# Optimization experiments

Measured on AMD Instinct MI355X. Metric: run time of the kernel, lower is better.

## Reference

```python
import jax, jax.numpy as jnp
import numpy as np

D_MODEL = 1024
N_HEADS = 16
HEAD_DIM = D_MODEL // N_HEADS
B, T = 4, 2048


def setup_inputs() -> dict:
    key = jax.random.key(0)
    ks = jax.random.split(key, 5)
    s = 1.0 / np.sqrt(D_MODEL)
    return {
        "x": jax.random.normal(ks[0], (B, T, D_MODEL), dtype=jnp.float32),
        "Wq": jax.random.normal(ks[1], (D_MODEL, D_MODEL), dtype=jnp.float32) * s,
        "bq": jnp.zeros((D_MODEL,), jnp.float32),
        "Wk": jax.random.normal(ks[2], (D_MODEL, D_MODEL), dtype=jnp.float32) * s,
        "bk": jnp.zeros((D_MODEL,), jnp.float32),
        "Wv": jax.random.normal(ks[3], (D_MODEL, D_MODEL), dtype=jnp.float32) * s,
        "bv": jnp.zeros((D_MODEL,), jnp.float32),
        "Wo": jax.random.normal(ks[4], (D_MODEL, D_MODEL), dtype=jnp.float32) * s,
        "bo": jnp.zeros((D_MODEL,), jnp.float32),
    }


def reference(x, Wq, bq, Wk, bk, Wv, bv, Wo, bo):
    Bx, Tx, C = x.shape
    H, Dh = N_HEADS, HEAD_DIM
    # projections (torch Linear: y = x @ W.T + b)
    q = (x @ Wq.T + bq).reshape(Bx, Tx, H, Dh).transpose(0, 2, 1, 3)  # [B,H,T,Dh]
    k = (x @ Wk.T + bk).reshape(Bx, Tx, H, Dh).transpose(0, 2, 1, 3)
    v = (x @ Wv.T + bv).reshape(Bx, Tx, H, Dh).transpose(0, 2, 1, 3)
    scores = jnp.einsum("bhqd,bhkd->bhqk", q, k) / np.sqrt(Dh).astype(np.float32)
    causal = jnp.tril(jnp.ones((Tx, Tx), dtype=bool))
    scores = jnp.where(causal, scores, -jnp.inf)
    attn = jax.nn.softmax(scores, axis=-1)  # dropout in eval mode = identity
    y = jnp.einsum("bhqk,bhkd->bhqd", attn, v)
    y = y.transpose(0, 2, 1, 3).reshape(Bx, Tx, C)
    return y @ Wo.T + bo
```

## Files before the change

### kernel.cpp

```cpp
#include <hip/hip_runtime.h>

typedef __attribute__((ext_vector_type(8))) short short8;
typedef __attribute__((ext_vector_type(4))) float f32x4;
typedef unsigned short u16;
typedef unsigned int u32;

#define NH 16

#if __has_builtin(__builtin_amdgcn_exp2f)
#define EXP2(x) __builtin_amdgcn_exp2f(x)
#else
#define EXP2(x) exp2f(x)
#endif

__device__ __forceinline__ u32 f2bf(float f) {
  u32 u = __builtin_bit_cast(u32, f);
  return (u + 0x7fffu + ((u >> 16) & 1u)) >> 16;
}

__global__ __launch_bounds__(256) void k_convert(
    const float* __restrict__ x, const float* __restrict__ wq,
    const float* __restrict__ wk, const float* __restrict__ wv,
    const float* __restrict__ wo, u16* __restrict__ dst) {
  int i = blockIdx.x * 256 + threadIdx.x;
  size_t e = (size_t)i * 4;
  const float* s; size_t off;
  if (e < 8388608ull)       { s = x;  off = e; }
  else if (e < 9437184ull)  { s = wq; off = e - 8388608ull; }
  else if (e < 10485760ull) { s = wk; off = e - 9437184ull; }
  else if (e < 11534336ull) { s = wv; off = e - 10485760ull; }
  else                      { s = wo; off = e - 11534336ull; }
  float4 d = *(const float4*)(s + off);
  ushort4 o;
  o.x = (u16)f2bf(d.x); o.y = (u16)f2bf(d.y);
  o.z = (u16)f2bf(d.z); o.w = (u16)f2bf(d.w);
  *(ushort4*)(dst + e) = o;
}

#define GEMM_CORE(Aptr, Bptr)                                                   \
  __shared__ u16 As[128 * 72];                                                  \
  __shared__ u16 Bs[128 * 72];                                                  \
  const int tid = threadIdx.x;                                                  \
  const int wave = tid >> 6, lane = tid & 63;                                   \
  const int wr = wave >> 1, wc = wave & 1;                                      \
  const int quad = lane >> 4, l16 = lane & 15;                                  \
  const int m0 = blockIdx.y * 128, n0 = blockIdx.x * 128;                       \
  f32x4 acc[4][4];                                                              \
  {                                                                             \
    f32x4 z = {0.f, 0.f, 0.f, 0.f};                                             \
    for (int a = 0; a < 4; ++a) for (int b2 = 0; b2 < 4; ++b2) acc[a][b2] = z;  \
  }                                                                             \
  for (int k0 = 0; k0 < 1024; k0 += 64) {                                       \
    _Pragma("unroll")                                                           \
    for (int i = 0; i < 4; ++i) {                                               \
      int c = i * 256 + tid;                                                    \
      int row = c >> 3, cc = c & 7;                                             \
      *(uint4*)(&As[row * 72 + cc * 8]) =                                       \
          *(const uint4*)(Aptr + (size_t)(m0 + row) * 1024 + k0 + cc * 8);      \
      *(uint4*)(&Bs[row * 72 + cc * 8]) =                                       \
          *(const uint4*)(Bptr + (size_t)(n0 + row) * 1024 + k0 + cc * 8);      \
    }                                                                           \
    __syncthreads();                                                            \
    _Pragma("unroll")                                                           \
    for (int ks = 0; ks < 2; ++ks) {                                            \
      short8 af[4], bfr[4];                                                     \
      _Pragma("unroll")                                                         \
      for (int t = 0; t < 4; ++t)                                               \
        af[t] = *(const short8*)(&As[(wr * 64 + t * 16 + l16) * 72 + ks * 32 + quad * 8]); \
      _Pragma("unroll")                                                         \
      for (int t = 0; t < 4; ++t)                                               \
        bfr[t] = *(const short8*)(&Bs[(wc * 64 + t * 16 + l16) * 72 + ks * 32 + quad * 8]); \
      _Pragma("unroll")                                                         \
      for (int mt = 0; mt < 4; ++mt) {                                          \
        _Pragma("unroll")                                                       \
        for (int nt = 0; nt < 4; ++nt)                                          \
          acc[mt][nt] = __builtin_amdgcn_mfma_f32_16x16x32_bf16(                \
              af[mt], bfr[nt], acc[mt][nt], 0, 0, 0);                           \
      }                                                                         \
    }                                                                           \
    __syncthreads();                                                            \
  }

__global__ __launch_bounds__(256, 2) void k_gemm_qkv(
    const u16* __restrict__ A, const u16* __restrict__ W,
    const float* __restrict__ bq, const float* __restrict__ bk,
    const float* __restrict__ bv, u16* __restrict__ qkv) {
  const int z = blockIdx.z;
  const u16* Bw = W + (size_t)z * 1048576;
  const float* bias = (z == 0) ? bq : (z == 1) ? bk : bv;
  u16* out = qkv + (size_t)z * 8388608;
  GEMM_CORE(A, Bw)
  const float scl = (z == 0) ? 0.125f * 1.44269504088896340736f : 1.0f;
  #pragma unroll
  for (int mt = 0; mt < 4; ++mt) {
    #pragma unroll
    for (int nt = 0; nt < 4; ++nt) {
      int n = n0 + wc * 64 + nt * 16 + l16;
      float bn = bias[n];
      int h = n >> 6, d = n & 63;
      #pragma unroll
      for (int r = 0; r < 4; ++r) {
        int m = m0 + wr * 64 + mt * 16 + quad * 4 + r;
        int b = m >> 11, t = m & 2047;
        float val = (acc[mt][nt][r] + bn) * scl;
        out[(((size_t)(b * NH + h) * 2048 + t) << 6) + d] = (u16)f2bf(val);
      }
    }
  }
}

__global__ __launch_bounds__(256, 2) void k_gemm_out(
    const u16* __restrict__ A, const u16* __restrict__ Bw,
    const float* __restrict__ bias, float* __restrict__ out) {
  GEMM_CORE(A, Bw)
  #pragma unroll
  for (int mt = 0; mt < 4; ++mt) {
    #pragma unroll
    for (int nt = 0; nt < 4; ++nt) {
      int n = n0 + wc * 64 + nt * 16 + l16;
      float bn = bias[n];
      #pragma unroll
      for (int r = 0; r < 4; ++r) {
        int m = m0 + wr * 64 + mt * 16 + quad * 4 + r;
        out[(size_t)m * 1024 + n] = acc[mt][nt][r] + bn;
      }
    }
  }
}

__global__ __launch_bounds__(256) void k_vtrans(const u16* __restrict__ v,
                                                u16* __restrict__ vt) {
  int t0 = blockIdx.x * 64;
  int bh = blockIdx.y;
  const u16* vs = v + (size_t)bh * 2048 * 64;
  u16* vd = vt + (size_t)bh * 64 * 2048;
  int tid = threadIdx.x;
  #pragma unroll
  for (int it = 0; it < 2; ++it) {
    int c = it * 256 + tid;
    int d = c >> 3, tc = c & 7;
    u16 tmp[8];
    #pragma unroll
    for (int j = 0; j < 8; ++j)
      tmp[j] = vs[(size_t)(t0 + tc * 8 + j) * 64 + d];
    uint4 pk;
    pk.x = (u32)tmp[0] | ((u32)tmp[1] << 16);
    pk.y = (u32)tmp[2] | ((u32)tmp[3] << 16);
    pk.z = (u32)tmp[4] | ((u32)tmp[5] << 16);
    pk.w = (u32)tmp[6] | ((u32)tmp[7] << 16);
    *(uint4*)(vd + (size_t)d * 2048 + t0 + tc * 8) = pk;
  }
}


#define ATTN_SUB(P, QF0, QF1, O, MI, LI, DIAG)                                 \
  {                                                                            \
    f32x4 st[4];                                                               \
    _Pragma("unroll")                                                          \
    for (int nt = 0; nt < 4; ++nt) {                                           \
      short8 kf0 = *(const short8*)(&Ks[P][(nt * 16 + l16) * 72 + quad * 8]);  \
      short8 kf1 = *(const short8*)(&Ks[P][(nt * 16 + l16) * 72 + 32 + quad * 8]); \
      f32x4 z4 = {0.f, 0.f, 0.f, 0.f};                                         \
      z4 = __builtin_amdgcn_mfma_f32_16x16x32_bf16(kf0, QF0, z4, 0, 0, 0);     \
      st[nt] = __builtin_amdgcn_mfma_f32_16x16x32_bf16(kf1, QF1, z4, 0, 0, 0); \
    }                                                                          \
    if (DIAG) {                                                                \
      int q_loc = wave * 16 + l16;                                             \
      _Pragma("unroll")                                                        \
      for (int nt = 0; nt < 4; ++nt) {                                         \
        _Pragma("unroll")                                                      \
        for (int r = 0; r < 4; ++r) {                                          \
          int k_loc = nt * 16 + quad * 4 + r;                                  \
          if (k_loc > q_loc) st[nt][r] = -1e30f;                               \
        }                                                                      \
      }                                                                        \
    }                                                                          \
    float mq[4];                                                               \
    _Pragma("unroll")                                                          \
    for (int nt = 0; nt < 4; ++nt)                                             \
      mq[nt] = fmaxf(fmaxf(st[nt][0], st[nt][1]), fmaxf(st[nt][2], st[nt][3]));\
    float mx = fmaxf(fmaxf(mq[0], mq[1]), fmaxf(mq[2], mq[3]));                \
    mx = fmaxf(mx, __shfl_xor(mx, 16, 64));                                    \
    mx = fmaxf(mx, __shfl_xor(mx, 32, 64));                                    \
    float mnew = fmaxf(MI, mx);                                                \
    float alpha = EXP2(MI - mnew);                                             \
    MI = mnew;                                                                 \
    LI *= alpha;                                                               \
    _Pragma("unroll")                                                          \
    for (int r = 0; r < 4; ++r) {                                              \
      float av = __shfl(alpha, quad * 4 + r, 16);                              \
      _Pragma("unroll")                                                        \
      for (int dt = 0; dt < 4; ++dt) O[dt][r] *= av;                           \
    }                                                                          \
    u32 Wx[4], Wy[4];                                                          \
    float sq[4];                                                               \
    _Pragma("unroll")                                                          \
    for (int nt = 0; nt < 4; ++nt) {                                           \
      float p0 = EXP2(st[nt][0] - mnew);                                       \
      float p1 = EXP2(st[nt][1] - mnew);                                       \
      float p2 = EXP2(st[nt][2] - mnew);                                       \
      float p3 = EXP2(st[nt][3] - mnew);                                       \
      sq[nt] = (p0 + p1) + (p2 + p3);                                          \
      Wx[nt] = f2bf(p0) | (f2bf(p1) << 16);                                    \
      Wy[nt] = f2bf(p2) | (f2bf(p3) << 16);                                    \
    }                                                                          \
    float sum = (sq[0] + sq[1]) + (sq[2] + sq[3]);                             \
    sum += __shfl_xor(sum, 16, 64);                                            \
    sum += __shfl_xor(sum, 32, 64);                                            \
    LI += sum;                                                                 \
    uint4 t0, t1;                                                              \
    {                                                                          \
      u32 e, f;                                                                \
      e = __shfl(Wx[0], s0, 64); f = __shfl(Wx[1], s0, 64); t0.x = hi ? f : e; \
      e = __shfl(Wy[0], s0, 64); f = __shfl(Wy[1], s0, 64); t0.y = hi ? f : e; \
      e = __shfl(Wx[0], s1, 64); f = __shfl(Wx[1], s1, 64); t0.z = hi ? f : e; \
      e = __shfl(Wy[0], s1, 64); f = __shfl(Wy[1], s1, 64); t0.w = hi ? f : e; \
      e = __shfl(Wx[2], s0, 64); f = __shfl(Wx[3], s0, 64); t1.x = hi ? f : e; \
      e = __shfl(Wy[2], s0, 64); f = __shfl(Wy[3], s0, 64); t1.y = hi ? f : e; \
      e = __shfl(Wx[2], s1, 64); f = __shfl(Wx[3], s1, 64); t1.z = hi ? f : e; \
      e = __shfl(Wy[2], s1, 64); f = __shfl(Wy[3], s1, 64); t1.w = hi ? f : e; \
    }                                                                          \
    short8 pf0 = __builtin_bit_cast(short8, t0);                               \
    short8 pf1 = __builtin_bit_cast(short8, t1);                               \
    _Pragma("unroll")                                                          \
    for (int dt = 0; dt < 4; ++dt) {                                           \
      short8 vf0 = *(const short8*)(&Vs[P][(dt * 16 + l16) * 72 + quad * 8]);  \
      short8 vf1 = *(const short8*)(&Vs[P][(dt * 16 + l16) * 72 + 32 + quad * 8]); \
      O[dt] = __builtin_amdgcn_mfma_f32_16x16x32_bf16(pf0, vf0, O[dt], 0, 0, 0); \
      O[dt] = __builtin_amdgcn_mfma_f32_16x16x32_bf16(pf1, vf1, O[dt], 0, 0, 0); \
    }                                                                          \
  }

#define ATTN_EPI(O, LI, QT)                                                    \
  _Pragma("unroll")                                                            \
  for (int r = 0; r < 4; ++r) {                                                \
    float lv = __shfl(LI, quad * 4 + r, 16);                                   \
    float inv = 1.0f / lv;                                                     \
    int t = (QT) * 64 + wave * 16 + quad * 4 + r;                              \
    _Pragma("unroll")                                                          \
    for (int dt = 0; dt < 4; ++dt) {                                           \
      int d = dt * 16 + l16;                                                   \
      y[(((size_t)b * 2048 + t) * NH + h) * 64 + d] = (u16)f2bf(O[dt][r] * inv); \
    }                                                                          \
  }

__global__ __launch_bounds__(256, 4) void k_attn(
    const u16* __restrict__ q, const u16* __restrict__ k,
    const u16* __restrict__ vt, u16* __restrict__ y) {
  const int tid = threadIdx.x;
  const int wave = tid >> 6, lane = tid & 63;
  const int quad = lane >> 4, l16 = lane & 15;
  const int bh = blockIdx.x, bx = blockIdx.y;
  const int qtB = bx, qtA = 31 - bx;
  const int b = bh >> 4, h = bh & 15;

  __shared__ u16 Ks[2][64 * 72];
  __shared__ u16 Vs[2][64 * 72];

  const u16* qbA = q + ((size_t)bh * 2048 + qtA * 64 + wave * 16 + l16) * 64;
  short8 qA0 = *(const short8*)(qbA + quad * 8);
  short8 qA1 = *(const short8*)(qbA + 32 + quad * 8);
  const u16* qbB = q + ((size_t)bh * 2048 + qtB * 64 + wave * 16 + l16) * 64;
  short8 qB0 = *(const short8*)(qbB + quad * 8);
  short8 qB1 = *(const short8*)(qbB + 32 + quad * 8);

  f32x4 oA[4], oB[4];
  {
    f32x4 z = {0.f, 0.f, 0.f, 0.f};
    #pragma unroll
    for (int dt = 0; dt < 4; ++dt) { oA[dt] = z; oB[dt] = z; }
  }
  float mA = -1e30f, lA = 0.f, mB = -1e30f, lB = 0.f;

  const u16* kbase = k + (size_t)bh * 131072;
  const u16* vbase = vt + (size_t)bh * 131072;
  const int r0 = tid >> 3, cc = tid & 7;
  const int s0 = ((quad & 1) << 5) + l16, s1 = s0 + 16;
  const int hi = quad >> 1;

  {
    uint4 k0 = *(const uint4*)(kbase + (size_t)r0 * 64 + cc * 8);
    uint4 k1 = *(const uint4*)(kbase + (size_t)(r0 + 32) * 64 + cc * 8);
    uint4 v0 = *(const uint4*)(vbase + (size_t)r0 * 2048 + cc * 8);
    uint4 v1 = *(const uint4*)(vbase + (size_t)(r0 + 32) * 2048 + cc * 8);
    *(uint4*)(&Ks[0][r0 * 72 + cc * 8]) = k0;
    *(uint4*)(&Ks[0][(r0 + 32) * 72 + cc * 8]) = k1;
    *(uint4*)(&Vs[0][r0 * 72 + cc * 8]) = v0;
    *(uint4*)(&Vs[0][(r0 + 32) * 72 + cc * 8]) = v1;
  }
  __syncthreads();

  for (int kt = 0; kt <= qtA; ++kt) {
    const int p = kt & 1;
    const bool pre = (kt < qtA);
    uint4 kr0, kr1, vr0, vr1;
    if (pre) {
      const u16* kb = kbase + (size_t)(kt + 1) * 4096;
      const u16* vb = vbase + (kt + 1) * 64;
      kr0 = *(const uint4*)(kb + (size_t)r0 * 64 + cc * 8);
      kr1 = *(const uint4*)(kb + (size_t)(r0 + 32) * 64 + cc * 8);
      vr0 = *(const uint4*)(vb + (size_t)r0 * 2048 + cc * 8);
      vr1 = *(const uint4*)(vb + (size_t)(r0 + 32) * 2048 + cc * 8);
    }

    ATTN_SUB(p, qA0, qA1, oA, mA, lA, (kt == qtA))
    if (kt <= qtB) {
      ATTN_SUB(p, qB0, qB1, oB, mB, lB, (kt == qtB))
    }

    if (pre) {
      *(uint4*)(&Ks[p ^ 1][r0 * 72 + cc * 8]) = kr0;
      *(uint4*)(&Ks[p ^ 1][(r0 + 32) * 72 + cc * 8]) = kr1;
      *(uint4*)(&Vs[p ^ 1][r0 * 72 + cc * 8]) = vr0;
      *(uint4*)(&Vs[p ^ 1][(r0 + 32) * 72 + cc * 8]) = vr1;
    }
    __syncthreads();
  }

  ATTN_EPI(oA, lA, qtA)
  ATTN_EPI(oB, lB, qtB)
}

extern "C" void kernel_launch(void* const* d_in, const int* in_sizes, int n_in,
                              void* d_out, int out_size, void* d_ws, size_t ws_size,
                              hipStream_t stream) {
  const float* x  = (const float*)d_in[0];
  const float* Wq = (const float*)d_in[1];
  const float* bq = (const float*)d_in[2];
  const float* Wk = (const float*)d_in[3];
  const float* bk = (const float*)d_in[4];
  const float* Wv = (const float*)d_in[5];
  const float* bv = (const float*)d_in[6];
  const float* Wo = (const float*)d_in[7];
  const float* bo = (const float*)d_in[8];
  float* out = (float*)d_out;

  u16* ws  = (u16*)d_ws;
  u16* xb  = ws;
  u16* Wb  = ws + 8388608;
  u16* qkv = ws + 12582912;
  u16* vt  = ws + 37748736;
  u16* y   = ws + 46137344;

  k_convert<<<dim3(12288), dim3(256), 0, stream>>>(x, Wq, Wk, Wv, Wo, ws);
  k_gemm_qkv<<<dim3(8, 64, 3), dim3(256), 0, stream>>>(xb, Wb, bq, bk, bv, qkv);
  k_vtrans<<<dim3(32, 64), dim3(256), 0, stream>>>(qkv + 2 * 8388608, vt);
  k_attn<<<dim3(64, 16), dim3(256), 0, stream>>>(qkv, qkv + 8388608, vt, y);
  k_gemm_out<<<dim3(8, 64), dim3(256), 0, stream>>>(y, Wb + 3 * 1048576, bo, out);
}
```

Before: 309.1 us.

## Rewrite projection GEMMs with 256x256 tiles, async LDS loads and double buffering

Replaces the 128x128 register-staged GEMM core with a 256x256-tile, 8-wave kernel. It uses global_load_lds direct-to-LDS copies, double-buffered shared memory, XOR-swizzled LDS layout, and interleaved barrier/setprio phases so loads overlap MFMA work. The QKV projection becomes one fused N=3072 GEMM with a grouped block-index swizzle for L2 reuse. The goal is to cut global-load latency stalls and LDS bank conflicts, at the cost of 128KB LDS per block and fewer blocks (128 for the output GEMM), which may underfill the GPU.

New measurement: 321.4 us. 4.0% more time.

```diff
diff --git a/kernel.cpp b/kernel.cpp
--- a/kernel.cpp
+++ b/kernel.cpp
@@ -16,6 +16,12 @@
 __device__ __forceinline__ u32 f2bf(float f) {
   u32 u = __builtin_bit_cast(u32, f);
   return (u + 0x7fffu + ((u >> 16) & 1u)) >> 16;
+}
+
+__device__ __forceinline__ void gload_lds16(const u16* g, u16* l) {
+  __builtin_amdgcn_global_load_lds(
+      (const __attribute__((address_space(1))) void*)g,
+      (__attribute__((address_space(3))) void*)l, 16, 0, 0);
 }
 
 __global__ __launch_bounds__(256) void k_convert(
@@ -37,91 +43,184 @@
   *(ushort4*)(dst + e) = o;
 }
 
-#define GEMM_CORE(Aptr, Bptr)                                                   \
-  __shared__ u16 As[128 * 72];                                                  \
-  __shared__ u16 Bs[128 * 72];                                                  \
-  const int tid = threadIdx.x;                                                  \
-  const int wave = tid >> 6, lane = tid & 63;                                   \
-  const int wr = wave >> 1, wc = wave & 1;                                      \
-  const int quad = lane >> 4, l16 = lane & 15;                                  \
-  const int m0 = blockIdx.y * 128, n0 = blockIdx.x * 128;                       \
-  f32x4 acc[4][4];                                                              \
-  {                                                                             \
-    f32x4 z = {0.f, 0.f, 0.f, 0.f};                                             \
-    for (int a = 0; a < 4; ++a) for (int b2 = 0; b2 < 4; ++b2) acc[a][b2] = z;  \
-  }                                                                             \
-  for (int k0 = 0; k0 < 1024; k0 += 64) {                                       \
-    _Pragma("unroll")                                                           \
-    for (int i = 0; i < 4; ++i) {                                               \
-      int c = i * 256 + tid;                                                    \
-      int row = c >> 3, cc = c & 7;                                             \
-      *(uint4*)(&As[row * 72 + cc * 8]) =                                       \
-          *(const uint4*)(Aptr + (size_t)(m0 + row) * 1024 + k0 + cc * 8);      \
-      *(uint4*)(&Bs[row * 72 + cc * 8]) =                                       \
-          *(const uint4*)(Bptr + (size_t)(n0 + row) * 1024 + k0 + cc * 8);      \
-    }                                                                           \
-    __syncthreads();                                                            \
-    _Pragma("unroll")                                                           \
-    for (int ks = 0; ks < 2; ++ks) {                                            \
-      short8 af[4], bfr[4];                                                     \
-      _Pragma("unroll")                                                         \
-      for (int t = 0; t < 4; ++t)                                               \
-        af[t] = *(const short8*)(&As[(wr * 64 + t * 16 + l16) * 72 + ks * 32 + quad * 8]); \
-      _Pragma("unroll")                                                         \
-      for (int t = 0; t < 4; ++t)                                               \
-        bfr[t] = *(const short8*)(&Bs[(wc * 64 + t * 16 + l16) * 72 + ks * 32 + quad * 8]); \
-      _Pragma("unroll")                                                         \
-      for (int mt = 0; mt < 4; ++mt) {                                          \
-        _Pragma("unroll")                                                       \
-        for (int nt = 0; nt < 4; ++nt)                                          \
-          acc[mt][nt] = __builtin_amdgcn_mfma_f32_16x16x32_bf16(                \
-              af[mt], bfr[nt], acc[mt][nt], 0, 0, 0);                           \
-      }                                                                         \
-    }                                                                           \
-    __syncthreads();                                                            \
-  }
-
-__global__ __launch_bounds__(256, 2) void k_gemm_qkv(
+#define GEMM256_CORE(Aptr, Bptr)                                               \
+  __shared__ u16 As[2][16384];                                                 \
+  __shared__ u16 Bs[2][16384];                                                 \
+  const int tid = threadIdx.x;                                                 \
+  const int wave = tid >> 6, lane = tid & 63;                                  \
+  const int quad = lane >> 4, l16 = lane & 15;                                 \
+  const int wr = wave >> 2, wn = wave & 3;                                     \
+  const int swz = l16 & 7;                                                     \
+  const int srow = tid >> 3;                                                   \
+  const int srcg = (tid & 7) ^ (srow & 7);                                     \
+  const u16* aTh = Aptr + (size_t)(m0 + srow) * 1024 + srcg * 8;               \
+  const u16* bTh = Bptr + (size_t)(n0 + srow) * 1024 + srcg * 8;               \
+  u16* aDst = &As[0][0] + wave * 512;                                          \
+  u16* bDst = &Bs[0][0] + wave * 512;                                          \
+  f32x4 acc[8][4];                                                             \
+  {                                                                            \
+    f32x4 z = {0.f, 0.f, 0.f, 0.f};                                            \
+    for (int a = 0; a < 8; ++a) for (int b2 = 0; b2 < 4; ++b2) acc[a][b2] = z; \
+  }                                                                            \
+  _Pragma("unroll")                                                            \
+  for (int j = 0; j < 4; ++j) {                                                \
+    gload_lds16(aTh + j * 65536, aDst + j * 4096);                             \
+    gload_lds16(bTh + j * 65536, bDst + j * 4096);                             \
+  }                                                                            \
+  __syncthreads();                                                             \
+  for (int t = 0; t < 16; ++t) {                                               \
+    const int p = t & 1;                                                       \
+    if (t < 15) {                                                              \
+      const u16* aT = aTh + (t + 1) * 64;                                      \
+      const u16* bT = bTh + (t + 1) * 64;                                      \
+      u16* aD = aDst + (p ^ 1) * 16384;                                        \
+      u16* bD = bDst + (p ^ 1) * 16384;                                        \
+      _Pragma("unroll")                                                        \
+      for (int j = 0; j < 4; ++j) {                                            \
+        gload_lds16(aT + j * 65536, aD + j * 4096);                            \
+        gload_lds16(bT + j * 65536, bD + j * 4096);                            \
+      }                                                                        \
+    }                                                                          \
+    __builtin_amdgcn_sched_barrier(0);                                         \
+    const u16* Ab = &As[p][0];                                                 \
+    const u16* Bb = &Bs[p][0];                                                 \
+    short8 af[4][2], bfr[2][2];                                                \
+                                                            \
+    _Pragma("unroll")                                                          \
+    for (int mt = 0; mt < 4; ++mt)                                             \
+      _Pragma("unroll")                                                        \
+      for (int ks = 0; ks < 2; ++ks)                                           \
+        af[mt][ks] = *(const short8*)(Ab + (wr * 128 + mt * 16 + l16) * 64     \
+                                         + ((ks * 4 + quad) ^ swz) * 8);       \
+    _Pragma("unroll")                                                          \
+    for (int nt = 0; nt < 2; ++nt)                                             \
+      _Pragma("unroll")                                                        \
+      for (int ks = 0; ks < 2; ++ks)                                           \
+        bfr[nt][ks] = *(const short8*)(Bb + (wn * 64 + nt * 16 + l16) * 64     \
+                                          + ((ks * 4 + quad) ^ swz) * 8);      \
+    __builtin_amdgcn_s_barrier();                                              \
+    __builtin_amdgcn_s_setprio(1);                                             \
+    _Pragma("unroll")                                                          \
+    for (int mt = 0; mt < 4; ++mt)                                             \
+      _Pragma("unroll")                                                        \
+      for (int nt = 0; nt < 2; ++nt)                                           \
+        _Pragma("unroll")                                                      \
+        for (int ks = 0; ks < 2; ++ks)                                         \
+          acc[mt][nt] = __builtin_amdgcn_mfma_f32_16x16x32_bf16(               \
+              af[mt][ks], bfr[nt][ks], acc[mt][nt], 0, 0, 0);                  \
+    __builtin_amdgcn_s_setprio(0);                                             \
+    __builtin_amdgcn_s_barrier();                                              \
+    __builtin_amdgcn_sched_barrier(0);                                         \
+                                                  \
+    _Pragma("unroll")                                                          \
+    for (int nt = 0; nt < 2; ++nt)                                             \
+      _Pragma("unroll")                                                        \
+      for (int ks = 0; ks < 2; ++ks)                                           \
+        bfr[nt][ks] = *(const short8*)(Bb + (wn * 64 + (nt + 2) * 16 + l16) * 64 \
+                                          + ((ks * 4 + quad) ^ swz) * 8);      \
+    __builtin_amdgcn_s_barrier();                                              \
+    __builtin_amdgcn_s_setprio(1);                                             \
+    _Pragma("unroll")                                                          \
+    for (int mt = 0; mt < 4; ++mt)                                             \
+      _Pragma("unroll")                                                        \
+      for (int nt = 0; nt < 2; ++nt)                                           \
+        _Pragma("unroll")                                                      \
+        for (int ks = 0; ks < 2; ++ks)                                         \
+          acc[mt][nt + 2] = __builtin_amdgcn_mfma_f32_16x16x32_bf16(           \
+              af[mt][ks], bfr[nt][ks], acc[mt][nt + 2], 0, 0, 0);              \
+    __builtin_amdgcn_s_setprio(0);                                             \
+    __builtin_amdgcn_s_barrier();                                              \
+    __builtin_amdgcn_sched_barrier(0);                                         \
+                                                 \
+    _Pragma("unroll")                                                          \
+    for (int mt = 0; mt < 4; ++mt)                                             \
+      _Pragma("unroll")                                                        \
+      for (int ks = 0; ks < 2; ++ks)                                           \
+        af[mt][ks] = *(const short8*)(Ab + (wr * 128 + (mt + 4) * 16 + l16) * 64 \
+                                         + ((ks * 4 + quad) ^ swz) * 8);       \
+    __builtin_amdgcn_s_barrier();                                              \
+    __builtin_amdgcn_s_setprio(1);                                             \
+    _Pragma("unroll")                                                          \
+    for (int mt = 0; mt < 4; ++mt)                                             \
+      _Pragma("unroll")                                                        \
+      for (int nt = 0; nt < 2; ++nt)                                           \
+        _Pragma("unroll")                                                      \
+        for (int ks = 0; ks < 2; ++ks)                                         \
+          acc[mt + 4][nt + 2] = __builtin_amdgcn_mfma_f32_16x16x32_bf16(       \
+              af[mt][ks], bfr[nt][ks], acc[mt + 4][nt + 2], 0, 0, 0);          \
+    __builtin_amdgcn_s_setprio(0);                                             \
+    __builtin_amdgcn_s_barrier();                                              \
+    __builtin_amdgcn_sched_barrier(0);                                         \
+                                          \
+    _Pragma("unroll")                                                          \
+    for (int nt = 0; nt < 2; ++nt)                                             \
+      _Pragma("unroll")                                                        \
+      for (int ks = 0; ks < 2; ++ks)                                           \
+        bfr[nt][ks] = *(const short8*)(Bb + (wn * 64 + nt * 16 + l16) * 64     \
+                                          + ((ks * 4 + quad) ^ swz) * 8);      \
+    __builtin_amdgcn_s_barrier();                                              \
+    __builtin_amdgcn_s_setprio(1);                                             \
+    _Pragma("unroll")                                                          \
+    for (int mt = 0; mt < 4; ++mt)                                             \
+      _Pragma("unroll")                                                        \
+      for (int nt = 0; nt < 2; ++nt)                                           \
+        _Pragma("unroll")                                                      \
+        for (int ks = 0; ks < 2; ++ks)                                         \
+          acc[mt + 4][nt] = __builtin_amdgcn_mfma_f32_16x16x32_bf16(           \
+              af[mt][ks], bfr[nt][ks], acc[mt + 4][nt], 0, 0, 0);              \
+    __builtin_amdgcn_s_setprio(0);                                             \
+    __syncthreads();                  \
+  }
+
+__global__ __launch_bounds__(512, 2) void k_gemm_qkv(
     const u16* __restrict__ A, const u16* __restrict__ W,
     const float* __restrict__ bq, const float* __restrict__ bk,
     const float* __restrict__ bv, u16* __restrict__ qkv) {
-  const int z = blockIdx.z;
-  const u16* Bw = W + (size_t)z * 1048576;
+  const int bid = blockIdx.x;
+  const int sw = (bid & 7) * 48 + (bid >> 3);
+  const int ntile = sw % 12, mtile = sw / 12;
+  const int m0 = mtile * 256, n0 = ntile * 256;
+  const int z = n0 >> 10;
   const float* bias = (z == 0) ? bq : (z == 1) ? bk : bv;
   u16* out = qkv + (size_t)z * 8388608;
-  GEMM_CORE(A, Bw)
   const float scl = (z == 0) ? 0.125f * 1.44269504088896340736f : 1.0f;
+  GEMM256_CORE(A, W)
   #pragma unroll
-  for (int mt = 0; mt < 4; ++mt) {
+  for (int mt = 0; mt < 8; ++mt) {
     #pragma unroll
     for (int nt = 0; nt < 4; ++nt) {
-      int n = n0 + wc * 64 + nt * 16 + l16;
-      float bn = bias[n];
-      int h = n >> 6, d = n & 63;
+      int n = n0 + wn * 64 + nt * 16 + l16;
+      int nn = n & 1023;
+      float bn = bias[nn];
+      int h = nn >> 6, d = nn & 63;
       #pragma unroll
       for (int r = 0; r < 4; ++r) {
-        int m = m0 + wr * 64 + mt * 16 + quad * 4 + r;
-        int b = m >> 11, t = m & 2047;
+        int m = m0 + wr * 128 + mt * 16 + quad * 4 + r;
+        int b = m >> 11, tt = m & 2047;
         float val = (acc[mt][nt][r] + bn) * scl;
-        out[(((size_t)(b * NH + h) * 2048 + t) << 6) + d] = (u16)f2bf(val);
+        out[(((size_t)(b * NH + h) * 2048 + tt) << 6) + d] = (u16)f2bf(val);
       }
     }
   }
 }
 
-__global__ __launch_bounds__(256, 2) void k_gemm_out(
+__global__ __launch_bounds__(512, 2) void k_gemm_out(
     const u16* __restrict__ A, const u16* __restrict__ Bw,
     const float* __restrict__ bias, float* __restrict__ out) {
-  GEMM_CORE(A, Bw)
+  const int bid = blockIdx.x;
+  const int sw = (bid & 7) * 16 + (bid >> 3);
+  const int ntile = sw % 4, mtile = sw / 4;
+  const int m0 = mtile * 256, n0 = ntile * 256;
+  GEMM256_CORE(A, Bw)
   #pragma unroll
-  for (int mt = 0; mt < 4; ++mt) {
+  for (int mt = 0; mt < 8; ++mt) {
     #pragma unroll
     for (int nt = 0; nt < 4; ++nt) {
-      int n = n0 + wc * 64 + nt * 16 + l16;
+      int n = n0 + wn * 64 + nt * 16 + l16;
       float bn = bias[n];
       #pragma unroll
       for (int r = 0; r < 4; ++r) {
-        int m = m0 + wr * 64 + mt * 16 + quad * 4 + r;
+        int m = m0 + wr * 128 + mt * 16 + quad * 4 + r;
         out[(size_t)m * 1024 + n] = acc[mt][nt][r] + bn;
       }
     }
@@ -152,7 +251,6 @@
   }
 }
 
-
 #define ATTN_SUB(P, QF0, QF1, O, MI, LI, DIAG)                                 \
   {                                                                            \
     f32x4 st[4];                                                               \
@@ -343,8 +441,8 @@
   u16* y   = ws + 46137344;
 
   k_convert<<<dim3(12288), dim3(256), 0, stream>>>(x, Wq, Wk, Wv, Wo, ws);
-  k_gemm_qkv<<<dim3(8, 64, 3), dim3(256), 0, stream>>>(xb, Wb, bq, bk, bv, qkv);
+  k_gemm_qkv<<<dim3(384), dim3(512), 0, stream>>>(xb, Wb, bq, bk, bv, qkv);
   k_vtrans<<<dim3(32, 64), dim3(256), 0, stream>>>(qkv + 2 * 8388608, vt);
   k_attn<<<dim3(64, 16), dim3(256), 0, stream>>>(qkv, qkv + 8388608, vt, y);
-  k_gemm_out<<<dim3(8, 64), dim3(256), 0, stream>>>(y, Wb + 3 * 1048576, bo, out);
-}
+  k_gemm_out<<<dim3(128), dim3(512), 0, stream>>>(y, Wb + 3 * 1048576, bo, out);
+}
```

## Rewrite projection GEMMs with direct-to-LDS double buffering and fuse V transpose

Applied to the files above, without the earlier changes.

Replaces the simple register-staged GEMM core with a template that loads tiles straight into LDS using global_load_lds. It double-buffers LDS with explicit vmcnt waits, uses XOR-swizzled layouts, larger 256-wide tiles with 512 threads, grouped block ordering and setprio around the MFMA phases. The QKV GEMM now writes V directly in transposed layout, so the separate transpose kernel is gone. The aim is to overlap global loads with MFMA work and cut a kernel launch, at the cost of more LDS and registers per block, which may lower occupancy.

After: 301.6 us. -2.5%, faster.

```diff
diff --git a/kernel.cpp b/kernel.cpp
--- a/kernel.cpp
+++ b/kernel.cpp
@@ -16,6 +16,12 @@
 __device__ __forceinline__ u32 f2bf(float f) {
   u32 u = __builtin_bit_cast(u32, f);
   return (u + 0x7fffu + ((u >> 16) & 1u)) >> 16;
+}
+
+__device__ __forceinline__ void gload_lds16(const u16* g, u16* l) {
+  __builtin_amdgcn_global_load_lds(
+      (const __attribute__((address_space(1))) void*)g,
+      (__attribute__((address_space(3))) void*)l, 16, 0, 0);
 }
 
 __global__ __launch_bounds__(256) void k_convert(
@@ -37,121 +43,191 @@
   *(ushort4*)(dst + e) = o;
 }
 
-#define GEMM_CORE(Aptr, Bptr)                                                   \
-  __shared__ u16 As[128 * 72];                                                  \
-  __shared__ u16 Bs[128 * 72];                                                  \
-  const int tid = threadIdx.x;                                                  \
-  const int wave = tid >> 6, lane = tid & 63;                                   \
-  const int wr = wave >> 1, wc = wave & 1;                                      \
-  const int quad = lane >> 4, l16 = lane & 15;                                  \
-  const int m0 = blockIdx.y * 128, n0 = blockIdx.x * 128;                       \
-  f32x4 acc[4][4];                                                              \
-  {                                                                             \
-    f32x4 z = {0.f, 0.f, 0.f, 0.f};                                             \
-    for (int a = 0; a < 4; ++a) for (int b2 = 0; b2 < 4; ++b2) acc[a][b2] = z;  \
-  }                                                                             \
-  for (int k0 = 0; k0 < 1024; k0 += 64) {                                       \
-    _Pragma("unroll")                                                           \
-    for (int i = 0; i < 4; ++i) {                                               \
-      int c = i * 256 + tid;                                                    \
-      int row = c >> 3, cc = c & 7;                                             \
-      *(uint4*)(&As[row * 72 + cc * 8]) =                                       \
-          *(const uint4*)(Aptr + (size_t)(m0 + row) * 1024 + k0 + cc * 8);      \
-      *(uint4*)(&Bs[row * 72 + cc * 8]) =                                       \
-          *(const uint4*)(Bptr + (size_t)(n0 + row) * 1024 + k0 + cc * 8);      \
-    }                                                                           \
-    __syncthreads();                                                            \
-    _Pragma("unroll")                                                           \
-    for (int ks = 0; ks < 2; ++ks) {                                            \
-      short8 af[4], bfr[4];                                                     \
-      _Pragma("unroll")                                                         \
-      for (int t = 0; t < 4; ++t)                                               \
-        af[t] = *(const short8*)(&As[(wr * 64 + t * 16 + l16) * 72 + ks * 32 + quad * 8]); \
-      _Pragma("unroll")                                                         \
-      for (int t = 0; t < 4; ++t)                                               \
-        bfr[t] = *(const short8*)(&Bs[(wc * 64 + t * 16 + l16) * 72 + ks * 32 + quad * 8]); \
-      _Pragma("unroll")                                                         \
-      for (int mt = 0; mt < 4; ++mt) {                                          \
-        _Pragma("unroll")                                                       \
-        for (int nt = 0; nt < 4; ++nt)                                          \
-          acc[mt][nt] = __builtin_amdgcn_mfma_f32_16x16x32_bf16(                \
-              af[mt], bfr[nt], acc[mt][nt], 0, 0, 0);                           \
-      }                                                                         \
-    }                                                                           \
-    __syncthreads();                                                            \
-  }
-
-__global__ __launch_bounds__(256, 2) void k_gemm_qkv(
+#define GPHASE(MH, NH_, LA, LB)                                                \
+  if (LA) {                                                                    \
+    _Pragma("unroll")                                                          \
+    for (int mt = 0; mt < 4; ++mt)                                             \
+      _Pragma("unroll")                                                        \
+      for (int ks = 0; ks < 2; ++ks)                                           \
+        af[mt][ks] = *(const short8*)(Ab +                                     \
+            (wr * MT * 16 + ((MH) * 4 + mt) * 16 + l16) * 64 +                 \
+            ((ks * 4 + quad) ^ swz) * 8);                                      \
+  }                                                                            \
+  if (LB) {                                                                    \
+    _Pragma("unroll")                                                          \
+    for (int nt = 0; nt < NH2; ++nt)                                           \
+      _Pragma("unroll")                                                        \
+      for (int ks = 0; ks < 2; ++ks)                                           \
+        bfr[nt][ks] = *(const short8*)(Bb +                                    \
+            (wn * NT * 16 + ((NH_) * NH2 + nt) * 16 + l16) * 64 +              \
+            ((ks * 4 + quad) ^ swz) * 8);                                      \
+  }                                                                            \
+  __builtin_amdgcn_s_barrier();                                                \
+  __builtin_amdgcn_s_setprio(1);                                               \
+  _Pragma("unroll")                                                            \
+  for (int mt = 0; mt < 4; ++mt)                                               \
+    _Pragma("unroll")                                                          \
+    for (int nt = 0; nt < NH2; ++nt)                                           \
+      _Pragma("unroll")                                                        \
+      for (int ks = 0; ks < 2; ++ks)                                           \
+        acc[(MH) * 4 + mt][(NH_) * NH2 + nt] =                                 \
+            __builtin_amdgcn_mfma_f32_16x16x32_bf16(                           \
+                af[mt][ks], bfr[nt][ks], acc[(MH) * 4 + mt][(NH_) * NH2 + nt], \
+                0, 0, 0);                                                      \
+  __builtin_amdgcn_s_setprio(0);                                               \
+  __builtin_amdgcn_s_barrier();                                                \
+  __builtin_amdgcn_sched_barrier(0);
+
+#define STAGE_T(T, PB)                                                         \
+  {                                                                            \
+    const u16* aT = aTh + (T) * 64;                                            \
+    const u16* bT = bTh + (T) * 64;                                            \
+    u16* aD = &As[PB][0] + dbase;                                              \
+    u16* bD = &Bs[PB][0] + dbase;                                              \
+    _Pragma("unroll")                                                          \
+    for (int j = 0; j < NLA; ++j) gload_lds16(aT + j * 65536, aD + j * 4096);  \
+    _Pragma("unroll")                                                          \
+    for (int j = 0; j < NLB; ++j) gload_lds16(bT + j * 65536, bD + j * 4096);  \
+  }
+
+template <int MT, int NT>
+__device__ __forceinline__ void gemm_core(const u16* __restrict__ Aptr,
+                                          const u16* __restrict__ Bptr,
+                                          int m0, int n0, f32x4 (&acc)[8][4]) {
+  constexpr int NLA = MT / 2;
+  constexpr int NLB = NT;
+  constexpr int NLD = NLA + NLB;
+  constexpr int NH2 = NT / 2;
+  __shared__ u16 As[2][MT * 32 * 64];
+  __shared__ u16 Bs[2][NT * 64 * 64];
+  const int tid = threadIdx.x;
+  const int wave = tid >> 6, lane = tid & 63;
+  const int quad = lane >> 4, l16 = lane & 15;
+  const int wr = wave >> 2, wn = wave & 3;
+  const int swz = l16 & 7;
+  const int srow = tid >> 3;
+  const int srcg = (tid & 7) ^ (srow & 7);
+  const u16* aTh = Aptr + (size_t)(m0 + srow) * 1024 + srcg * 8;
+  const u16* bTh = Bptr + (size_t)(n0 + srow) * 1024 + srcg * 8;
+  const int dbase = wave * 512;
+
+  {
+    f32x4 z = {0.f, 0.f, 0.f, 0.f};
+    #pragma unroll
+    for (int a = 0; a < 8; ++a)
+      #pragma unroll
+      for (int b2 = 0; b2 < 4; ++b2) acc[a][b2] = z;
+  }
+
+  STAGE_T(0, 0)
+
+  short8 af[4][2], bfr[NH2][2];
+  for (int t = 0; t < 16; ++t) {
+    const int p = t & 1;
+    if (t < 15) {
+      STAGE_T(t + 1, p ^ 1)
+      if constexpr (NLD == 8)
+        asm volatile("s_waitcnt vmcnt(8)" ::: "memory");
+      else if constexpr (NLD == 6)
+        asm volatile("s_waitcnt vmcnt(6)" ::: "memory");
+      else
+        asm volatile("s_waitcnt vmcnt(0)" ::: "memory");
+    } else {
+      asm volatile("s_waitcnt vmcnt(0)" ::: "memory");
+    }
+    __builtin_amdgcn_s_barrier();
+    __builtin_amdgcn_sched_barrier(0);
+    const u16* Ab = &As[p][0];
+    const u16* Bb = &Bs[p][0];
+    GPHASE(0, 0, true, true)
+    GPHASE(0, 1, false, true)
+    GPHASE(1, 1, true, false)
+    GPHASE(1, 0, false, true)
+  }
+}
+
+__global__ __launch_bounds__(512, 2) void k_gemm_qkv(
     const u16* __restrict__ A, const u16* __restrict__ W,
     const float* __restrict__ bq, const float* __restrict__ bk,
-    const float* __restrict__ bv, u16* __restrict__ qkv) {
-  const int z = blockIdx.z;
-  const u16* Bw = W + (size_t)z * 1048576;
+    const float* __restrict__ bv, u16* __restrict__ qkv,
+    u16* __restrict__ vt) {
+  const int bid = blockIdx.x;
+  const int sw = (bid & 7) * 48 + (bid >> 3);
+  const int ntile = sw % 12, mtile = sw / 12;
+  const int m0 = mtile * 256, n0 = ntile * 256;
+  const int z = n0 >> 10;
   const float* bias = (z == 0) ? bq : (z == 1) ? bk : bv;
   u16* out = qkv + (size_t)z * 8388608;
-  GEMM_CORE(A, Bw)
   const float scl = (z == 0) ? 0.125f * 1.44269504088896340736f : 1.0f;
-  #pragma unroll
-  for (int mt = 0; mt < 4; ++mt) {
+  f32x4 acc[8][4];
+  gemm_core<8, 4>(A, W, m0, n0, acc);
+  const int tid = threadIdx.x;
+  const int wave = tid >> 6, lane = tid & 63;
+  const int quad = lane >> 4, l16 = lane & 15;
+  const int wr = wave >> 2, wn = wave & 3;
+  if (z == 2) {
     #pragma unroll
-    for (int nt = 0; nt < 4; ++nt) {
-      int n = n0 + wc * 64 + nt * 16 + l16;
-      float bn = bias[n];
-      int h = n >> 6, d = n & 63;
+    for (int mt = 0; mt < 8; ++mt) {
       #pragma unroll
-      for (int r = 0; r < 4; ++r) {
-        int m = m0 + wr * 64 + mt * 16 + quad * 4 + r;
-        int b = m >> 11, t = m & 2047;
-        float val = (acc[mt][nt][r] + bn) * scl;
-        out[(((size_t)(b * NH + h) * 2048 + t) << 6) + d] = (u16)f2bf(val);
+      for (int nt = 0; nt < 4; ++nt) {
+        int nn = (n0 + wn * 64 + nt * 16 + l16) & 1023;
+        float bn = bias[nn];
+        int h = nn >> 6, d = nn & 63;
+        int mbase = m0 + wr * 128 + mt * 16 + quad * 4;
+        int b = mbase >> 11, tb = mbase & 2047;
+        uint2 pk;
+        pk.x = f2bf(acc[mt][nt][0] + bn) | (f2bf(acc[mt][nt][1] + bn) << 16);
+        pk.y = f2bf(acc[mt][nt][2] + bn) | (f2bf(acc[mt][nt][3] + bn) << 16);
+        *(uint2*)(vt + ((size_t)(b * NH + h) * 64 + d) * 2048 + tb) = pk;
       }
     }
-  }
-}
-
-__global__ __launch_bounds__(256, 2) void k_gemm_out(
+  } else {
+    #pragma unroll
+    for (int mt = 0; mt < 8; ++mt) {
+      #pragma unroll
+      for (int nt = 0; nt < 4; ++nt) {
+        int nn = (n0 + wn * 64 + nt * 16 + l16) & 1023;
+        float bn = bias[nn];
+        int h = nn >> 6, d = nn & 63;
+        #pragma unroll
+        for (int r = 0; r < 4; ++r) {
+          int m = m0 + wr * 128 + mt * 16 + quad * 4 + r;
+          int b = m >> 11, tt = m & 2047;
+          float val = (acc[mt][nt][r] + bn) * scl;
+          out[(((size_t)(b * NH + h) * 2048 + tt) << 6) + d] = (u16)f2bf(val);
+        }
+      }
+    }
+  }
+}
+
+__global__ __launch_bounds__(512, 2) void k_gemm_out(
     const u16* __restrict__ A, const u16* __restrict__ Bw,
     const float* __restrict__ bias, float* __restrict__ out) {
-  GEMM_CORE(A, Bw)
+  const int bid = blockIdx.x;
+  const int sw = (bid & 7) * 32 + (bid >> 3);
+  const int mtile = sw >> 3, ntile = sw & 7;
+  const int m0 = mtile * 256, n0 = ntile * 128;
+  f32x4 acc[8][4];
+  gemm_core<8, 2>(A, Bw, m0, n0, acc);
+  const int tid = threadIdx.x;
+  const int wave = tid >> 6, lane = tid & 63;
+  const int quad = lane >> 4, l16 = lane & 15;
+  const int wr = wave >> 2, wn = wave & 3;
   #pragma unroll
-  for (int mt = 0; mt < 4; ++mt) {
+  for (int mt = 0; mt < 8; ++mt) {
     #pragma unroll
-    for (int nt = 0; nt < 4; ++nt) {
-      int n = n0 + wc * 64 + nt * 16 + l16;
+    for (int nt = 0; nt < 2; ++nt) {
+      int n = n0 + wn * 32 + nt * 16 + l16;
       float bn = bias[n];
       #pragma unroll
       for (int r = 0; r < 4; ++r) {
-        int m = m0 + wr * 64 + mt * 16 + quad * 4 + r;
+        int m = m0 + wr * 128 + mt * 16 + quad * 4 + r;
         out[(size_t)m * 1024 + n] = acc[mt][nt][r] + bn;
       }
     }
   }
 }
-
-__global__ __launch_bounds__(256) void k_vtrans(const u16* __restrict__ v,
-                                                u16* __restrict__ vt) {
-  int t0 = blockIdx.x * 64;
-  int bh = blockIdx.y;
-  const u16* vs = v + (size_t)bh * 2048 * 64;
-  u16* vd = vt + (size_t)bh * 64 * 2048;
-  int tid = threadIdx.x;
-  #pragma unroll
-  for (int it = 0; it < 2; ++it) {
-    int c = it * 256 + tid;
-    int d = c >> 3, tc = c & 7;
-    u16 tmp[8];
-    #pragma unroll
-    for (int j = 0; j < 8; ++j)
-      tmp[j] = vs[(size_t)(t0 + tc * 8 + j) * 64 + d];
-    uint4 pk;
-    pk.x = (u32)tmp[0] | ((u32)tmp[1] << 16);
-    pk.y = (u32)tmp[2] | ((u32)tmp[3] << 16);
-    pk.z = (u32)tmp[4] | ((u32)tmp[5] << 16);
-    pk.w = (u32)tmp[6] | ((u32)tmp[7] << 16);
-    *(uint4*)(vd + (size_t)d * 2048 + t0 + tc * 8) = pk;
-  }
-}
-
 
 #define ATTN_SUB(P, QF0, QF1, O, MI, LI, DIAG)                                 \
   {                                                                            \
@@ -343,8 +419,7 @@
   u16* y   = ws + 46137344;
 
   k_convert<<<dim3(12288), dim3(256), 0, stream>>>(x, Wq, Wk, Wv, Wo, ws);
-  k_gemm_qkv<<<dim3(8, 64, 3), dim3(256), 0, stream>>>(xb, Wb, bq, bk, bv, qkv);
-  k_vtrans<<<dim3(32, 64), dim3(256), 0, stream>>>(qkv + 2 * 8388608, vt);
+  k_gemm_qkv<<<dim3(384), dim3(512), 0, stream>>>(xb, Wb, bq, bk, bv, qkv, vt);
   k_attn<<<dim3(64, 16), dim3(256), 0, stream>>>(qkv, qkv + 8388608, vt, y);
-  k_gemm_out<<<dim3(8, 64), dim3(256), 0, stream>>>(y, Wb + 3 * 1048576, bo, out);
-}
+  k_gemm_out<<<dim3(256), dim3(512), 0, stream>>>(y, Wb + 3 * 1048576, bo, out);
+}
```
